# Kernel optimization log

Hardware: AMD Instinct MI355X
Metric: run time of the kernel (lower is better)

## Reference

```python
import jax, jax.numpy as jnp
import numpy as np

WS = 3  # window size


def _shift_stack(t_pad, D, H, W):
    # t_pad: [B, nh, hd, D+2p, H+2p, W+2p] -> [B, nh, hd, D, H, W, WS**3]
    slabs = [t_pad[..., i:i + D, j:j + H, l:l + W]
             for i in range(WS) for j in range(WS) for l in range(WS)]
    return jnp.stack(slabs, axis=-1)


def setup_inputs() -> dict:
    key = jax.random.key(0)
    ks = jax.random.split(key, 6)
    B, C, D, H, W = 2, 128, 24, 24, 24
    nh, hd = 4, 32
    return {
        "x": jax.random.normal(ks[0], (B, C, D, H, W), dtype=jnp.float32),
        "qkv_w": jax.random.normal(ks[1], (3 * C, C), dtype=jnp.float32) * 0.02,
        "qkv_b": jax.random.normal(ks[2], (3 * C,), dtype=jnp.float32) * 0.02,
        "proj_w": jax.random.normal(ks[3], (C, C), dtype=jnp.float32) * 0.02,
        "proj_b": jax.random.normal(ks[4], (C,), dtype=jnp.float32) * 0.02,
        "pos_embed": jax.random.normal(ks[5], (hd, WS, WS, WS), dtype=jnp.float32) * 0.02,
    }


def reference(x, qkv_w, qkv_b, proj_w, proj_b, pos_embed):
    B, C, D, H, W = x.shape
    hd = pos_embed.shape[0]
    nh = C // hd
    scale = hd ** -0.5
    pad = WS // 2

    # 1x1x1 Conv3d == pointwise linear over channel dim
    qkv = jnp.einsum('bcdhw,oc->bodhw', x, qkv_w) + qkv_b[None, :, None, None, None]
    q, k, v = jnp.split(qkv, 3, axis=1)
    q = q.reshape(B, nh, hd, D, H, W)
    k = k.reshape(B, nh, hd, D, H, W)
    v = v.reshape(B, nh, hd, D, H, W)

    pcfg = [(0, 0)] * 3 + [(pad, pad)] * 3
    k_pad = jnp.pad(k, pcfg)
    v_pad = jnp.pad(v, pcfg)

    # windows: [B, nh, hd, D, H, W, WS^3]; window center of q == q itself
    k_win = _shift_stack(k_pad, D, H, W)
    v_win = _shift_stack(v_pad, D, H, W)
    k_win = k_win + pos_embed.reshape(hd, WS ** 3)[None, None, :, None, None, None, :]

    scores = jnp.einsum('bncdhw,bncdhwk->bndhwk', q, k_win) * scale
    attn = jax.nn.softmax(scores, axis=-1)
    out = jnp.einsum('bndhwk,bncdhwk->bncdhw', attn, v_win)
    out = out.reshape(B, C, D, H, W)
    return jnp.einsum('bcdhw,oc->bodhw', out, proj_w) + proj_b[None, :, None, None, None]
```

## Files before the change

### kernel.cpp

```cpp
#include <hip/hip_runtime.h>
#include <hip/hip_bf16.h>

#define SVOX 13824
#define CIN 128
#define NHEAD 4
#define HDIM 32

#define BD 2
#define BH 4
#define BW 8
#define WD (BD+2)
#define WH (BH+2)
#define WW (BW+2)
#define NWIN (WD*WH*WW)

typedef __attribute__((ext_vector_type(8))) short short8;
typedef __attribute__((ext_vector_type(4))) float f32x4;
#if defined(__has_builtin)
#if __has_builtin(__builtin_amdgcn_fdot2_f32_bf16)
#define HAVE_DOT2BF 1
typedef __attribute__((ext_vector_type(2))) __bf16 bf16x2;
#endif
#if __has_builtin(__builtin_amdgcn_mov_dpp)
#define HAVE_DPP 1
#endif
#endif

__device__ __forceinline__ unsigned short f2bf(float x) {
    unsigned u = __float_as_uint(x);
    u += 0x7FFFu + ((u >> 16) & 1u);
    return (unsigned short)(u >> 16);
}
__device__ __forceinline__ float dot2bf(unsigned a, unsigned b, float c) {
#ifdef HAVE_DOT2BF
    return __builtin_amdgcn_fdot2_f32_bf16(__builtin_bit_cast(bf16x2, a),
                                           __builtin_bit_cast(bf16x2, b), c, false);
#else
    return __uint_as_float(a << 16) * __uint_as_float(b << 16)
         + __uint_as_float(a & 0xffff0000u) * __uint_as_float(b & 0xffff0000u) + c;
#endif
}
template<int CTRL>
__device__ __forceinline__ float quad_dpp(float x) {
#ifdef HAVE_DPP
    return __int_as_float(__builtin_amdgcn_mov_dpp(__float_as_int(x), CTRL, 0xf, 0xf, true));
#else
    return __shfl_xor(x, (CTRL == 0xB1) ? 1 : 2);
#endif
}

__global__ __launch_bounds__(256) void qkv_gemm(
    const float* __restrict__ X,
    const float* __restrict__ W,
    const float* __restrict__ bias,
    const float* __restrict__ pos,
    unsigned* __restrict__ pe_out,
    ushort* __restrict__ q_out,
    ushort* __restrict__ k_out,
    ushort* __restrict__ v_out)
{
    __shared__ __align__(16) unsigned char smem[26624];
    ushort* Wb = (ushort*)smem;
    ushort* Xs = (ushort*)(smem + 17408);
    float*  T  = (float*)smem;

    const int t    = threadIdx.x;
    const int s0   = blockIdx.x * 64;
    const int o0   = blockIdx.y * 64;
    const int b    = blockIdx.z;
    const int lane = t & 63;
    const int wid  = t >> 6;
    const int l15  = lane & 15;
    const int g4   = lane >> 4;
    const int wm   = (wid >> 1) * 32;
    const int wn   = (wid & 1) * 32;

    if (blockIdx.x == 0 && blockIdx.y == 0 && blockIdx.z == 0 && t < 27 * 16) {
        int w = t >> 4, cp = t & 15;
        unsigned lo = f2bf(pos[(2 * cp) * 27 + w]);
        unsigned hi = f2bf(pos[(2 * cp + 1) * 27 + w]);
        pe_out[t] = lo | (hi << 16);
    }

    #pragma unroll
    for (int i = 0; i < 8; i++) {
        int f = t + i * 256;
        int row = f >> 5, c4 = f & 31;
        float4 w = *(const float4*)(W + (size_t)(o0 + row) * CIN + c4 * 4);
        ushort4 u;
        u.x = f2bf(w.x); u.y = f2bf(w.y); u.z = f2bf(w.z); u.w = f2bf(w.w);
        *(ushort4*)(Wb + row * 136 + c4 * 4) = u;
    }

    f32x4 acc[2][2];
    #pragma unroll
    for (int mf = 0; mf < 2; mf++)
        #pragma unroll
        for (int nf = 0; nf < 2; nf++)
            acc[mf][nf] = (f32x4){0.f, 0.f, 0.f, 0.f};

    const int sx = t & 63;
    const int kg = t >> 6;

    for (int chunk = 0; chunk < 2; chunk++) {
        __syncthreads();
        ushort xk[16];
        #pragma unroll
        for (int i = 0; i < 16; i++) {
            int k = kg * 16 + i;
            xk[i] = f2bf(X[((size_t)b * CIN + chunk * 64 + k) * SVOX + s0 + sx]);
        }
        #pragma unroll
        for (int j = 0; j < 2; j++) {
            short8 v;
            #pragma unroll
            for (int e = 0; e < 8; e++) v[e] = (short)xk[j * 8 + e];
            *(short8*)(Xs + sx * 72 + kg * 16 + j * 8) = v;
        }
        __syncthreads();

        #pragma unroll
        for (int ks = 0; ks < 2; ks++) {
            short8 Af[2], Bf[2];
            #pragma unroll
            for (int mf = 0; mf < 2; mf++)
                Af[mf] = *(const short8*)(Wb + (wm + mf * 16 + l15) * 136 + chunk * 64 + ks * 32 + g4 * 8);
            #pragma unroll
            for (int nf = 0; nf < 2; nf++)
                Bf[nf] = *(const short8*)(Xs + (wn + nf * 16 + l15) * 72 + ks * 32 + g4 * 8);
            #pragma unroll
            for (int mf = 0; mf < 2; mf++)
                #pragma unroll
                for (int nf = 0; nf < 2; nf++)
                    acc[mf][nf] = __builtin_amdgcn_mfma_f32_16x16x32_bf16(Af[mf], Bf[nf], acc[mf][nf], 0, 0, 0);
        }
    }

    __syncthreads();
    #pragma unroll
    for (int mf = 0; mf < 2; mf++)
        #pragma unroll
        for (int nf = 0; nf < 2; nf++) {
            int s  = wn + nf * 16 + l15;
            int mb = wm + mf * 16 + g4 * 4;
            *(f32x4*)(T + s * 68 + mb) = acc[mf][nf];
        }
    __syncthreads();
    #pragma unroll
    for (int i = 0; i < 4; i++) {
        int f = t + i * 256;
        int og = f & 15, sl = f >> 4;
        float4 v = *(float4*)(T + sl * 68 + og * 4);
        int o_g = o0 + og * 4;
        v.x += bias[o_g]; v.y += bias[o_g + 1]; v.z += bias[o_g + 2]; v.w += bias[o_g + 3];
        int part = o_g >> 7, pc = o_g & 127;
        int head = pc >> 5, ic = pc & 31;
        size_t base = (((size_t)b * NHEAD + head) * SVOX + s0 + sl) * HDIM + ic;
        ushort4 u;
        u.x = f2bf(v.x); u.y = f2bf(v.y); u.z = f2bf(v.z); u.w = f2bf(v.w);
        ushort* dst = (part == 0) ? q_out : (part == 1) ? k_out : v_out;
        *(ushort4*)(dst + base) = u;
    }
}

__global__ __launch_bounds__(256, 5) void attn_kernel(
    const ushort* __restrict__ qbf,
    const ushort* __restrict__ kbf,
    const ushort* __restrict__ vbf,
    const unsigned* __restrict__ pe_g,
    ushort* __restrict__ aout)
{
    __shared__ __align__(16) ushort Kl[NWIN * 32];
    __shared__ __align__(16) ushort Vl[NWIN * 32];

    const int t = threadIdx.x;
    const int br = blockIdx.x;
    const int n  = blockIdx.y;
    const int b  = blockIdx.z;
    const int bw_ = br % 3;
    const int bh_ = (br / 3) % 6;
    const int bd_ = br / 18;
    const int d0 = bd_ * BD, h0 = bh_ * BH, w0 = bw_ * BW;

    const ushort* kb = kbf + ((size_t)b * NHEAD + n) * (size_t)SVOX * HDIM;
    const ushort* vb = vbf + ((size_t)b * NHEAD + n) * (size_t)SVOX * HDIM;

    #pragma unroll
    for (int i = 0; i < 4; i++) {
        int f = t + i * 256;
        if (f < NWIN * 4) {
            int u = f >> 2, ch = f & 3;
            int ud = u / (WH * WW);
            int r  = u - ud * (WH * WW);
            int uh = r / WW;
            int uw = r - uh * WW;
            int gd = d0 + ud - 1, gh = h0 + uh - 1, gw = w0 + uw - 1;
            bool valid = ((unsigned)gd < 24u) & ((unsigned)gh < 24u) & ((unsigned)gw < 24u);
            size_t gsv = valid ? (size_t)(gd * 576 + gh * 24 + gw) : 0;
            uint4 kv = *(const uint4*)(kb + gsv * HDIM + ch * 8);
            uint4 vv = *(const uint4*)(vb + gsv * HDIM + ch * 8);
            if (!valid) { kv = make_uint4(0,0,0,0); vv = make_uint4(0,0,0,0); }
            *(uint4*)(Kl + u * 32 + ch * 8) = kv;
            *(uint4*)(Vl + u * 32 + ch * 8) = vv;
        }
    }

    const int p   = t >> 2;
    const int sub = t & 3;
    const int pw = p & 7, ph = (p >> 3) & 3, pd = p >> 5;
    const int dd0 = d0 + pd, hh0 = h0 + ph, ww0 = w0 + pw;
    const int sv = dd0 * 576 + hh0 * 24 + ww0;
    uint4 qpk = *(const uint4*)(qbf + (((size_t)b * NHEAD + n) * SVOX + sv) * HDIM + sub * 8);

    unsigned vm = 0;
    {
        int widx = 0;
        #pragma unroll
        for (int di = -1; di <= 1; di++)
        #pragma unroll
        for (int dj = -1; dj <= 1; dj++)
        #pragma unroll
        for (int dl = -1; dl <= 1; dl++) {
            if (((unsigned)(dd0 + di) < 24u) & ((unsigned)(hh0 + dj) < 24u) & ((unsigned)(ww0 + dl) < 24u))
                vm |= 1u << widx;
            widx++;
        }
    }
    (void)vm;

    float sc[27];
    #pragma unroll
    for (int s = 0; s < 27; s++) {
        uint4 pp = *(const uint4*)(pe_g + s * 16 + sub * 4);
        float a = dot2bf(qpk.x, pp.x, 0.f);
        a = dot2bf(qpk.y, pp.y, a);
        a = dot2bf(qpk.z, pp.z, a);
        a = dot2bf(qpk.w, pp.w, a);
        sc[s] = a;
    }

    __syncthreads();

    const int wc = (pd + 1) * (WH * WW) + (ph + 1) * WW + (pw + 1);
    const ushort* Kbase = Kl + wc * 32 + sub * 8;

    #pragma unroll
    for (int s = 0; s < 27; s++) {
        const int di = s / 9 - 1, dj = (s / 3) % 3 - 1, dl = s % 3 - 1;
        const int off = (di * (WH * WW) + dj * WW + dl) * 32;
        uint4 kk = *(const uint4*)(Kbase + off);
        float a = sc[s];
        a = dot2bf(qpk.x, kk.x, a);
        a = dot2bf(qpk.y, kk.y, a);
        a = dot2bf(qpk.z, kk.z, a);
        a = dot2bf(qpk.w, kk.w, a);
        sc[s] = a;
    }

    #pragma unroll
    for (int s = 0; s < 27; s++) {
        sc[s] += quad_dpp<0xB1>(sc[s]);
        sc[s] += quad_dpp<0x4E>(sc[s]);
    }

    const float scale = 0.17677669529663687f;
    float mx = -1e30f;
    #pragma unroll
    for (int s = 0; s < 27; s++) {
        sc[s] *= scale;
        mx = fmaxf(mx, sc[s]);
    }
    float sum = 0.f;
    #pragma unroll
    for (int s = 0; s < 27; s++) {
        float e = __expf(sc[s] - mx);
        sc[s] = e;
        sum += e;
    }
    float inv = 1.f / sum;

    const ushort* Vbase = Vl + wc * 32 + sub * 8;
    float o[8];
    #pragma unroll
    for (int i = 0; i < 8; i++) o[i] = 0.f;
    #pragma unroll
    for (int s = 0; s < 27; s++) {
        const int di = s / 9 - 1, dj = (s / 3) % 3 - 1, dl = s % 3 - 1;
        const int off = (di * (WH * WW) + dj * WW + dl) * 32;
        uint4 vv = *(const uint4*)(Vbase + off);
        float pr = sc[s];
        o[0] += pr * __uint_as_float(vv.x << 16);
        o[1] += pr * __uint_as_float(vv.x & 0xffff0000u);
        o[2] += pr * __uint_as_float(vv.y << 16);
        o[3] += pr * __uint_as_float(vv.y & 0xffff0000u);
        o[4] += pr * __uint_as_float(vv.z << 16);
        o[5] += pr * __uint_as_float(vv.z & 0xffff0000u);
        o[6] += pr * __uint_as_float(vv.w << 16);
        o[7] += pr * __uint_as_float(vv.w & 0xffff0000u);
    }

    uint4 ou;
    ou.x = (unsigned)f2bf(o[0] * inv) | ((unsigned)f2bf(o[1] * inv) << 16);
    ou.y = (unsigned)f2bf(o[2] * inv) | ((unsigned)f2bf(o[3] * inv) << 16);
    ou.z = (unsigned)f2bf(o[4] * inv) | ((unsigned)f2bf(o[5] * inv) << 16);
    ou.w = (unsigned)f2bf(o[6] * inv) | ((unsigned)f2bf(o[7] * inv) << 16);
    *(uint4*)(aout + ((size_t)b * SVOX + sv) * CIN + n * HDIM + sub * 8) = ou;
}

__global__ __launch_bounds__(256) void proj_gemm(
    const ushort* __restrict__ Xa,
    const float* __restrict__ W,
    const float* __restrict__ bias,
    float* __restrict__ out)
{
    __shared__ __align__(16) unsigned char smem[34816];
    ushort* Wb = (ushort*)smem;
    ushort* Xs = (ushort*)(smem + 17408);
    float*  T  = (float*)smem;

    const int t    = threadIdx.x;
    const int s0   = blockIdx.x * 64;
    const int o0   = blockIdx.y * 64;
    const int b    = blockIdx.z;
    const int lane = t & 63;
    const int wid  = t >> 6;
    const int l15  = lane & 15;
    const int g4   = lane >> 4;
    const int wm   = (wid >> 1) * 32;
    const int wn   = (wid & 1) * 32;

    #pragma unroll
    for (int i = 0; i < 8; i++) {
        int f = t + i * 256;
        int row = f >> 5, c4 = f & 31;
        float4 w = *(const float4*)(W + (size_t)(o0 + row) * CIN + c4 * 4);
        ushort4 u;
        u.x = f2bf(w.x); u.y = f2bf(w.y); u.z = f2bf(w.z); u.w = f2bf(w.w);
        *(ushort4*)(Wb + row * 136 + c4 * 4) = u;
    }
    #pragma unroll
    for (int i = 0; i < 4; i++) {
        int f = t + i * 256;
        int row = f >> 4, c8 = f & 15;
        *(uint4*)(Xs + row * 136 + c8 * 8) =
            *(const uint4*)(Xa + ((size_t)b * SVOX + s0 + row) * CIN + c8 * 8);
    }
    __syncthreads();

    f32x4 acc[2][2];
    #pragma unroll
    for (int mf = 0; mf < 2; mf++)
        #pragma unroll
        for (int nf = 0; nf < 2; nf++)
            acc[mf][nf] = (f32x4){0.f, 0.f, 0.f, 0.f};

    #pragma unroll
    for (int ks = 0; ks < 4; ks++) {
        short8 Af[2], Bf[2];
        #pragma unroll
        for (int mf = 0; mf < 2; mf++)
            Af[mf] = *(const short8*)(Wb + (wm + mf * 16 + l15) * 136 + ks * 32 + g4 * 8);
        #pragma unroll
        for (int nf = 0; nf < 2; nf++)
            Bf[nf] = *(const short8*)(Xs + (wn + nf * 16 + l15) * 136 + ks * 32 + g4 * 8);
        #pragma unroll
        for (int mf = 0; mf < 2; mf++)
            #pragma unroll
            for (int nf = 0; nf < 2; nf++)
                acc[mf][nf] = __builtin_amdgcn_mfma_f32_16x16x32_bf16(Af[mf], Bf[nf], acc[mf][nf], 0, 0, 0);
    }

    __syncthreads();
    #pragma unroll
    for (int mf = 0; mf < 2; mf++)
        #pragma unroll
        for (int nf = 0; nf < 2; nf++) {
            int s  = wn + nf * 16 + l15;
            int mb = wm + mf * 16 + g4 * 4;
            #pragma unroll
            for (int r = 0; r < 4; r++)
                T[(mb + r) * 72 + s] = acc[mf][nf][r];
        }
    __syncthreads();
    #pragma unroll
    for (int i = 0; i < 4; i++) {
        int f = t + i * 256;
        int s4 = f & 15, m = f >> 4;
        float4 v = *(float4*)(T + m * 72 + s4 * 4);
        float bi = bias[o0 + m];
        v.x += bi; v.y += bi; v.z += bi; v.w += bi;
        *(float4*)(out + ((size_t)b * CIN + o0 + m) * SVOX + s0 + s4 * 4) = v;
    }
}

extern "C" void kernel_launch(void* const* d_in, const int* in_sizes, int n_in,
                              void* d_out, int out_size, void* d_ws, size_t ws_size,
                              hipStream_t stream) {
    const float* x      = (const float*)d_in[0];
    const float* qkv_w  = (const float*)d_in[1];
    const float* qkv_b  = (const float*)d_in[2];
    const float* proj_w = (const float*)d_in[3];
    const float* proj_b = (const float*)d_in[4];
    const float* pos    = (const float*)d_in[5];
    float* out = (float*)d_out;

    const size_t HSZ = (size_t)2 * NHEAD * SVOX * HDIM;
    ushort* qb  = (ushort*)d_ws;
    ushort* kbp = qb + HSZ;
    ushort* vbp = kbp + HSZ;
    ushort* attn_o = vbp + HSZ;
    unsigned* pe_p = (unsigned*)(attn_o + HSZ);

    qkv_gemm<<<dim3(SVOX/64, 384/64, 2), 256, 0, stream>>>(x, qkv_w, qkv_b, pos, pe_p, qb, kbp, vbp);
    attn_kernel<<<dim3(216, NHEAD, 2), 256, 0, stream>>>(qb, kbp, vbp, pe_p, attn_o);
    proj_gemm<<<dim3(SVOX/64, CIN/64, 2), 256, 0, stream>>>(attn_o, proj_w, proj_b, out);
}
```

Baseline: 46.94 us.

## Pre-convert weights to bf16 once and enlarge GEMM output tiles

Adds a prep kernel that converts the qkv and proj weights and the positional embedding to bf16 once, so the GEMM blocks copy bf16 weights directly instead of each converting fp32. The qkv GEMM now computes 192 output channels per block (grid y drops from 6 to 2), so each X tile is loaded and converted fewer times. The proj GEMM now covers 128 voxels per block. In exchange it adds an extra kernel launch and much more LDS per block (60KB for qkv), which lowers occupancy and cuts the block count.

```diff
diff --git a/kernel.cpp b/kernel.cpp
--- a/kernel.cpp
+++ b/kernel.cpp
@@ -49,54 +49,76 @@
 #endif
 }
 
+__global__ __launch_bounds__(256) void prep_kernel(
+    const float* __restrict__ qkv_w,
+    const float* __restrict__ proj_w,
+    const float* __restrict__ pos,
+    ushort* __restrict__ Wq,
+    ushort* __restrict__ Wp,
+    unsigned* __restrict__ pe)
+{
+    int id = blockIdx.x * 256 + threadIdx.x;
+    if (id < 6144) {
+        float4 a = *(const float4*)(qkv_w + (size_t)id * 8);
+        float4 b = *(const float4*)(qkv_w + (size_t)id * 8 + 4);
+        ushort4 u, v;
+        u.x = f2bf(a.x); u.y = f2bf(a.y); u.z = f2bf(a.z); u.w = f2bf(a.w);
+        v.x = f2bf(b.x); v.y = f2bf(b.y); v.z = f2bf(b.z); v.w = f2bf(b.w);
+        *(ushort4*)(Wq + (size_t)id * 8) = u;
+        *(ushort4*)(Wq + (size_t)id * 8 + 4) = v;
+    } else if (id < 8192) {
+        int j = id - 6144;
+        float4 a = *(const float4*)(proj_w + (size_t)j * 8);
+        float4 b = *(const float4*)(proj_w + (size_t)j * 8 + 4);
+        ushort4 u, v;
+        u.x = f2bf(a.x); u.y = f2bf(a.y); u.z = f2bf(a.z); u.w = f2bf(a.w);
+        v.x = f2bf(b.x); v.y = f2bf(b.y); v.z = f2bf(b.z); v.w = f2bf(b.w);
+        *(ushort4*)(Wp + (size_t)j * 8) = u;
+        *(ushort4*)(Wp + (size_t)j * 8 + 4) = v;
+    } else if (id < 8192 + 432) {
+        int j = id - 8192;
+        int w = j >> 4, cp = j & 15;
+        unsigned lo = f2bf(pos[(2 * cp) * 27 + w]);
+        unsigned hi = f2bf(pos[(2 * cp + 1) * 27 + w]);
+        pe[j] = lo | (hi << 16);
+    }
+}
+
 __global__ __launch_bounds__(256) void qkv_gemm(
     const float* __restrict__ X,
-    const float* __restrict__ W,
+    const ushort* __restrict__ Wg,
     const float* __restrict__ bias,
-    const float* __restrict__ pos,
-    unsigned* __restrict__ pe_out,
     ushort* __restrict__ q_out,
     ushort* __restrict__ k_out,
     ushort* __restrict__ v_out)
 {
-    __shared__ __align__(16) unsigned char smem[26624];
+    __shared__ __align__(16) unsigned char smem[61440];
     ushort* Wb = (ushort*)smem;
-    ushort* Xs = (ushort*)(smem + 17408);
+    ushort* Xs = (ushort*)(smem + 52224);
     float*  T  = (float*)smem;
 
     const int t    = threadIdx.x;
     const int s0   = blockIdx.x * 64;
-    const int o0   = blockIdx.y * 64;
+    const int o0   = blockIdx.y * 192;
     const int b    = blockIdx.z;
     const int lane = t & 63;
     const int wid  = t >> 6;
     const int l15  = lane & 15;
     const int g4   = lane >> 4;
-    const int wm   = (wid >> 1) * 32;
-    const int wn   = (wid & 1) * 32;
-
-    if (blockIdx.x == 0 && blockIdx.y == 0 && blockIdx.z == 0 && t < 27 * 16) {
-        int w = t >> 4, cp = t & 15;
-        unsigned lo = f2bf(pos[(2 * cp) * 27 + w]);
-        unsigned hi = f2bf(pos[(2 * cp + 1) * 27 + w]);
-        pe_out[t] = lo | (hi << 16);
-    }
-
-    #pragma unroll
-    for (int i = 0; i < 8; i++) {
+
+    #pragma unroll
+    for (int i = 0; i < 12; i++) {
         int f = t + i * 256;
-        int row = f >> 5, c4 = f & 31;
-        float4 w = *(const float4*)(W + (size_t)(o0 + row) * CIN + c4 * 4);
-        ushort4 u;
-        u.x = f2bf(w.x); u.y = f2bf(w.y); u.z = f2bf(w.z); u.w = f2bf(w.w);
-        *(ushort4*)(Wb + row * 136 + c4 * 4) = u;
-    }
-
-    f32x4 acc[2][2];
-    #pragma unroll
-    for (int mf = 0; mf < 2; mf++)
-        #pragma unroll
-        for (int nf = 0; nf < 2; nf++)
+        int row = f >> 4, c8 = f & 15;
+        *(uint4*)(Wb + row * 136 + c8 * 8) =
+            *(const uint4*)(Wg + (size_t)(o0 + row) * CIN + c8 * 8);
+    }
+
+    f32x4 acc[3][4];
+    #pragma unroll
+    for (int mf = 0; mf < 3; mf++)
+        #pragma unroll
+        for (int nf = 0; nf < 4; nf++)
             acc[mf][nf] = (f32x4){0.f, 0.f, 0.f, 0.f};
 
     const int sx = t & 63;
@@ -121,45 +143,43 @@
 
         #pragma unroll
         for (int ks = 0; ks < 2; ks++) {
-            short8 Af[2], Bf[2];
-            #pragma unroll
-            for (int mf = 0; mf < 2; mf++)
-                Af[mf] = *(const short8*)(Wb + (wm + mf * 16 + l15) * 136 + chunk * 64 + ks * 32 + g4 * 8);
-            #pragma unroll
-            for (int nf = 0; nf < 2; nf++)
-                Bf[nf] = *(const short8*)(Xs + (wn + nf * 16 + l15) * 72 + ks * 32 + g4 * 8);
-            #pragma unroll
-            for (int mf = 0; mf < 2; mf++)
+            short8 Bf[4], Af[3];
+            #pragma unroll
+            for (int nf = 0; nf < 4; nf++)
+                Bf[nf] = *(const short8*)(Xs + (nf * 16 + l15) * 72 + ks * 32 + g4 * 8);
+            #pragma unroll
+            for (int mf = 0; mf < 3; mf++)
+                Af[mf] = *(const short8*)(Wb + (mf * 64 + wid * 16 + l15) * 136 + chunk * 64 + ks * 32 + g4 * 8);
+            #pragma unroll
+            for (int mf = 0; mf < 3; mf++)
                 #pragma unroll
-                for (int nf = 0; nf < 2; nf++)
+                for (int nf = 0; nf < 4; nf++)
                     acc[mf][nf] = __builtin_amdgcn_mfma_f32_16x16x32_bf16(Af[mf], Bf[nf], acc[mf][nf], 0, 0, 0);
         }
     }
 
-    __syncthreads();
-    #pragma unroll
-    for (int mf = 0; mf < 2; mf++)
-        #pragma unroll
-        for (int nf = 0; nf < 2; nf++) {
-            int s  = wn + nf * 16 + l15;
-            int mb = wm + mf * 16 + g4 * 4;
-            *(f32x4*)(T + s * 68 + mb) = acc[mf][nf];
-        }
-    __syncthreads();
-    #pragma unroll
-    for (int i = 0; i < 4; i++) {
-        int f = t + i * 256;
-        int og = f & 15, sl = f >> 4;
-        float4 v = *(float4*)(T + sl * 68 + og * 4);
-        int o_g = o0 + og * 4;
-        v.x += bias[o_g]; v.y += bias[o_g + 1]; v.z += bias[o_g + 2]; v.w += bias[o_g + 3];
-        int part = o_g >> 7, pc = o_g & 127;
-        int head = pc >> 5, ic = pc & 31;
-        size_t base = (((size_t)b * NHEAD + head) * SVOX + s0 + sl) * HDIM + ic;
-        ushort4 u;
-        u.x = f2bf(v.x); u.y = f2bf(v.y); u.z = f2bf(v.z); u.w = f2bf(v.w);
-        ushort* dst = (part == 0) ? q_out : (part == 1) ? k_out : v_out;
-        *(ushort4*)(dst + base) = u;
+    #pragma unroll
+    for (int p = 0; p < 3; p++) {
+        __syncthreads();
+        #pragma unroll
+        for (int nf = 0; nf < 4; nf++)
+            *(f32x4*)(T + (nf * 16 + l15) * 68 + wid * 16 + g4 * 4) = acc[p][nf];
+        __syncthreads();
+        #pragma unroll
+        for (int i = 0; i < 4; i++) {
+            int f = t + i * 256;
+            int og = f & 15, sl = f >> 4;
+            float4 v = *(float4*)(T + sl * 68 + og * 4);
+            int o_g = o0 + p * 64 + og * 4;
+            v.x += bias[o_g]; v.y += bias[o_g + 1]; v.z += bias[o_g + 2]; v.w += bias[o_g + 3];
+            int part = o_g >> 7, pc = o_g & 127;
+            int head = pc >> 5, ic = pc & 31;
+            size_t base = (((size_t)b * NHEAD + head) * SVOX + s0 + sl) * HDIM + ic;
+            ushort4 u;
+            u.x = f2bf(v.x); u.y = f2bf(v.y); u.z = f2bf(v.z); u.w = f2bf(v.w);
+            ushort* dst = (part == 0) ? q_out : (part == 1) ? k_out : v_out;
+            *(ushort4*)(dst + base) = u;
+        }
     }
 }
 
@@ -212,22 +232,6 @@
     const int sv = dd0 * 576 + hh0 * 24 + ww0;
     uint4 qpk = *(const uint4*)(qbf + (((size_t)b * NHEAD + n) * SVOX + sv) * HDIM + sub * 8);
 
-    unsigned vm = 0;
-    {
-        int widx = 0;
-        #pragma unroll
-        for (int di = -1; di <= 1; di++)
-        #pragma unroll
-        for (int dj = -1; dj <= 1; dj++)
-        #pragma unroll
-        for (int dl = -1; dl <= 1; dl++) {
-            if (((unsigned)(dd0 + di) < 24u) & ((unsigned)(hh0 + dj) < 24u) & ((unsigned)(ww0 + dl) < 24u))
-                vm |= 1u << widx;
-            widx++;
-        }
-    }
-    (void)vm;
-
     float sc[27];
     #pragma unroll
     for (int s = 0; s < 27; s++) {
@@ -309,37 +313,35 @@
 
 __global__ __launch_bounds__(256) void proj_gemm(
     const ushort* __restrict__ Xa,
-    const float* __restrict__ W,
+    const ushort* __restrict__ Wg,
     const float* __restrict__ bias,
     float* __restrict__ out)
 {
-    __shared__ __align__(16) unsigned char smem[34816];
+    __shared__ __align__(16) unsigned char smem[52224];
     ushort* Wb = (ushort*)smem;
     ushort* Xs = (ushort*)(smem + 17408);
     float*  T  = (float*)smem;
 
     const int t    = threadIdx.x;
-    const int s0   = blockIdx.x * 64;
+    const int s0   = blockIdx.x * 128;
     const int o0   = blockIdx.y * 64;
     const int b    = blockIdx.z;
     const int lane = t & 63;
     const int wid  = t >> 6;
     const int l15  = lane & 15;
     const int g4   = lane >> 4;
-    const int wm   = (wid >> 1) * 32;
-    const int wn   = (wid & 1) * 32;
-
+    const int wo   = (wid & 1) * 32;
+    const int ws   = (wid >> 1) * 64;
+
+    #pragma unroll
+    for (int i = 0; i < 4; i++) {
+        int f = t + i * 256;
+        int row = f >> 4, c8 = f & 15;
+        *(uint4*)(Wb + row * 136 + c8 * 8) =
+            *(const uint4*)(Wg + (size_t)(o0 + row) * CIN + c8 * 8);
+    }
     #pragma unroll
     for (int i = 0; i < 8; i++) {
-        int f = t + i * 256;
-        int row = f >> 5, c4 = f & 31;
-        float4 w = *(const float4*)(W + (size_t)(o0 + row) * CIN + c4 * 4);
-        ushort4 u;
-        u.x = f2bf(w.x); u.y = f2bf(w.y); u.z = f2bf(w.z); u.w = f2bf(w.w);
-        *(ushort4*)(Wb + row * 136 + c4 * 4) = u;
-    }
-    #pragma unroll
-    for (int i = 0; i < 4; i++) {
         int f = t + i * 256;
         int row = f >> 4, c8 = f & 15;
         *(uint4*)(Xs + row * 136 + c8 * 8) =
@@ -347,26 +349,26 @@
     }
     __syncthreads();
 
-    f32x4 acc[2][2];
+    f32x4 acc[2][4];
     #pragma unroll
     for (int mf = 0; mf < 2; mf++)
         #pragma unroll
-        for (int nf = 0; nf < 2; nf++)
+        for (int nf = 0; nf < 4; nf++)
             acc[mf][nf] = (f32x4){0.f, 0.f, 0.f, 0.f};
 
     #pragma unroll
     for (int ks = 0; ks < 4; ks++) {
-        short8 Af[2], Bf[2];
+        short8 Af[2], Bf[4];
         #pragma unroll
         for (int mf = 0; mf < 2; mf++)
-            Af[mf] = *(const short8*)(Wb + (wm + mf * 16 + l15) * 136 + ks * 32 + g4 * 8);
-        #pragma unroll
-        for (int nf = 0; nf < 2; nf++)
-            Bf[nf] = *(const short8*)(Xs + (wn + nf * 16 + l15) * 136 + ks * 32 + g4 * 8);
+            Af[mf] = *(const short8*)(Wb + (wo + mf * 16 + l15) * 136 + ks * 32 + g4 * 8);
+        #pragma unroll
+        for (int nf = 0; nf < 4; nf++)
+            Bf[nf] = *(const short8*)(Xs + (ws + nf * 16 + l15) * 136 + ks * 32 + g4 * 8);
         #pragma unroll
         for (int mf = 0; mf < 2; mf++)
             #pragma unroll
-            for (int nf = 0; nf < 2; nf++)
+            for (int nf = 0; nf < 4; nf++)
                 acc[mf][nf] = __builtin_amdgcn_mfma_f32_16x16x32_bf16(Af[mf], Bf[nf], acc[mf][nf], 0, 0, 0);
     }
 
@@ -374,19 +376,19 @@
     #pragma unroll
     for (int mf = 0; mf < 2; mf++)
         #pragma unroll
-        for (int nf = 0; nf < 2; nf++) {
-            int s  = wn + nf * 16 + l15;
-            int mb = wm + mf * 16 + g4 * 4;
+        for (int nf = 0; nf < 4; nf++) {
+            int s  = ws + nf * 16 + l15;
+            int mb = wo + mf * 16 + g4 * 4;
             #pragma unroll
             for (int r = 0; r < 4; r++)
-                T[(mb + r) * 72 + s] = acc[mf][nf][r];
+                T[(mb + r) * 132 + s] = acc[mf][nf][r];
         }
     __syncthreads();
     #pragma unroll
-    for (int i = 0; i < 4; i++) {
+    for (int i = 0; i < 8; i++) {
         int f = t + i * 256;
-        int s4 = f & 15, m = f >> 4;
-        float4 v = *(float4*)(T + m * 72 + s4 * 4);
+        int s4 = f & 31, m = f >> 5;
+        float4 v = *(float4*)(T + m * 132 + s4 * 4);
         float bi = bias[o0 + m];
         v.x += bi; v.y += bi; v.z += bi; v.w += bi;
         *(float4*)(out + ((size_t)b * CIN + o0 + m) * SVOX + s0 + s4 * 4) = v;
@@ -409,9 +411,12 @@
     ushort* kbp = qb + HSZ;
     ushort* vbp = kbp + HSZ;
     ushort* attn_o = vbp + HSZ;
-    unsigned* pe_p = (unsigned*)(attn_o + HSZ);
-
-    qkv_gemm<<<dim3(SVOX/64, 384/64, 2), 256, 0, stream>>>(x, qkv_w, qkv_b, pos, pe_p, qb, kbp, vbp);
+    ushort* Wq  = attn_o + HSZ;
+    ushort* Wp  = Wq + 384 * CIN;
+    unsigned* pe_p = (unsigned*)(Wp + CIN * CIN);
+
+    prep_kernel<<<34, 256, 0, stream>>>(qkv_w, proj_w, pos, Wq, Wp, pe_p);
+    qkv_gemm<<<dim3(SVOX/64, 2, 2), 256, 0, stream>>>(x, Wq, qkv_b, qb, kbp, vbp);
     attn_kernel<<<dim3(216, NHEAD, 2), 256, 0, stream>>>(qb, kbp, vbp, pe_p, attn_o);
-    proj_gemm<<<dim3(SVOX/64, CIN/64, 2), 256, 0, stream>>>(attn_o, proj_w, proj_b, out);
-}
+    proj_gemm<<<dim3(SVOX/128, 2, 2), 256, 0, stream>>>(attn_o, Wp, proj_b, out);
+}
```

Measured after the change: 49.89 us. +6.3%, slower.

## Store V in fp16 and accumulate attention output with packed half FMAs

Applied to the files above, without the earlier changes.

The QKV GEMM now writes V as fp16 instead of bf16, and the attention kernel accumulates P·V with packed __hfma2 on half2 registers instead of unpacking bf16 to fp32 and doing scalar FMAs. This roughly halves the ALU work in the PV loop. Softmax is also restructured: a tree max reduction and exp2f with the scale folded into the log2e constant, and an unused validity mask is removed. Accumulating in fp16 lowers precision and risks overflow if V values are large.

```diff
diff --git a/kernel.cpp b/kernel.cpp
--- a/kernel.cpp
+++ b/kernel.cpp
@@ -1,5 +1,6 @@
 #include <hip/hip_runtime.h>
 #include <hip/hip_bf16.h>
+#include <hip/hip_fp16.h>
 
 #define SVOX 13824
 #define CIN 128
@@ -24,6 +25,9 @@
 #if __has_builtin(__builtin_amdgcn_mov_dpp)
 #define HAVE_DPP 1
 #endif
+#if __has_builtin(__builtin_amdgcn_cvt_pkrtz)
+#define HAVE_PKRTZ 1
+#endif
 #endif
 
 __device__ __forceinline__ unsigned short f2bf(float x) {
@@ -47,6 +51,20 @@
 #else
     return __shfl_xor(x, (CTRL == 0xB1) ? 1 : 2);
 #endif
+}
+__device__ __forceinline__ __half2 u2h2(unsigned u) {
+    union { unsigned u; __half2 h; } c; c.u = u; return c.h;
+}
+__device__ __forceinline__ __half2 splat_h2(float x) {
+#ifdef HAVE_PKRTZ
+    auto v = __builtin_amdgcn_cvt_pkrtz(x, x);
+    union { decltype(v) a; __half2 h; } c; c.a = v; return c.h;
+#else
+    return __float2half2_rn(x);
+#endif
+}
+__device__ __forceinline__ unsigned short f2h(float x) {
+    return __builtin_bit_cast(unsigned short, (_Float16)x);
 }
 
 __global__ __launch_bounds__(256) void qkv_gemm(
@@ -157,7 +175,11 @@
         int head = pc >> 5, ic = pc & 31;
         size_t base = (((size_t)b * NHEAD + head) * SVOX + s0 + sl) * HDIM + ic;
         ushort4 u;
-        u.x = f2bf(v.x); u.y = f2bf(v.y); u.z = f2bf(v.z); u.w = f2bf(v.w);
+        if (part == 2) {
+            u.x = f2h(v.x); u.y = f2h(v.y); u.z = f2h(v.z); u.w = f2h(v.w);
+        } else {
+            u.x = f2bf(v.x); u.y = f2bf(v.y); u.z = f2bf(v.z); u.w = f2bf(v.w);
+        }
         ushort* dst = (part == 0) ? q_out : (part == 1) ? k_out : v_out;
         *(ushort4*)(dst + base) = u;
     }
@@ -166,7 +188,7 @@
 __global__ __launch_bounds__(256, 5) void attn_kernel(
     const ushort* __restrict__ qbf,
     const ushort* __restrict__ kbf,
-    const ushort* __restrict__ vbf,
+    const ushort* __restrict__ vhf,
     const unsigned* __restrict__ pe_g,
     ushort* __restrict__ aout)
 {
@@ -183,7 +205,7 @@
     const int d0 = bd_ * BD, h0 = bh_ * BH, w0 = bw_ * BW;
 
     const ushort* kb = kbf + ((size_t)b * NHEAD + n) * (size_t)SVOX * HDIM;
-    const ushort* vb = vbf + ((size_t)b * NHEAD + n) * (size_t)SVOX * HDIM;
+    const ushort* vb = vhf + ((size_t)b * NHEAD + n) * (size_t)SVOX * HDIM;
 
     #pragma unroll
     for (int i = 0; i < 4; i++) {
@@ -208,25 +230,8 @@
     const int p   = t >> 2;
     const int sub = t & 3;
     const int pw = p & 7, ph = (p >> 3) & 3, pd = p >> 5;
-    const int dd0 = d0 + pd, hh0 = h0 + ph, ww0 = w0 + pw;
-    const int sv = dd0 * 576 + hh0 * 24 + ww0;
+    const int sv = (d0 + pd) * 576 + (h0 + ph) * 24 + w0 + pw;
     uint4 qpk = *(const uint4*)(qbf + (((size_t)b * NHEAD + n) * SVOX + sv) * HDIM + sub * 8);
-
-    unsigned vm = 0;
-    {
-        int widx = 0;
-        #pragma unroll
-        for (int di = -1; di <= 1; di++)
-        #pragma unroll
-        for (int dj = -1; dj <= 1; dj++)
-        #pragma unroll
-        for (int dl = -1; dl <= 1; dl++) {
-            if (((unsigned)(dd0 + di) < 24u) & ((unsigned)(hh0 + dj) < 24u) & ((unsigned)(ww0 + dl) < 24u))
-                vm |= 1u << widx;
-            widx++;
-        }
-    }
-    (void)vm;
 
     float sc[27];
     #pragma unroll
@@ -263,40 +268,46 @@
         sc[s] += quad_dpp<0x4E>(sc[s]);
     }
 
-    const float scale = 0.17677669529663687f;
-    float mx = -1e30f;
+    float m3[9];
+    #pragma unroll
+    for (int j = 0; j < 9; j++)
+        m3[j] = fmaxf(fmaxf(sc[3*j], sc[3*j+1]), sc[3*j+2]);
+    float m9a = fmaxf(fmaxf(m3[0], m3[1]), m3[2]);
+    float m9b = fmaxf(fmaxf(m3[3], m3[4]), m3[5]);
+    float m9c = fmaxf(fmaxf(m3[6], m3[7]), m3[8]);
+    float mx  = fmaxf(fmaxf(m9a, m9b), m9c);
+
+    const float KS = 0.17677669529663687f * 1.4426950408889634f;
+    float sum = 0.f;
     #pragma unroll
     for (int s = 0; s < 27; s++) {
-        sc[s] *= scale;
-        mx = fmaxf(mx, sc[s]);
-    }
-    float sum = 0.f;
-    #pragma unroll
-    for (int s = 0; s < 27; s++) {
-        float e = __expf(sc[s] - mx);
+        float e = exp2f((sc[s] - mx) * KS);
         sc[s] = e;
         sum += e;
     }
     float inv = 1.f / sum;
 
     const ushort* Vbase = Vl + wc * 32 + sub * 8;
-    float o[8];
-    #pragma unroll
-    for (int i = 0; i < 8; i++) o[i] = 0.f;
+    __half2 o2[4];
+    __half2 hz = __float2half2_rn(0.f);
+    o2[0] = hz; o2[1] = hz; o2[2] = hz; o2[3] = hz;
     #pragma unroll
     for (int s = 0; s < 27; s++) {
         const int di = s / 9 - 1, dj = (s / 3) % 3 - 1, dl = s % 3 - 1;
         const int off = (di * (WH * WW) + dj * WW + dl) * 32;
         uint4 vv = *(const uint4*)(Vbase + off);
-        float pr = sc[s];
-        o[0] += pr * __uint_as_float(vv.x << 16);
-        o[1] += pr * __uint_as_float(vv.x & 0xffff0000u);
-        o[2] += pr * __uint_as_float(vv.y << 16);
-        o[3] += pr * __uint_as_float(vv.y & 0xffff0000u);
-        o[4] += pr * __uint_as_float(vv.z << 16);
-        o[5] += pr * __uint_as_float(vv.z & 0xffff0000u);
-        o[6] += pr * __uint_as_float(vv.w << 16);
-        o[7] += pr * __uint_as_float(vv.w & 0xffff0000u);
+        __half2 p2 = splat_h2(sc[s]);
+        o2[0] = __hfma2(p2, u2h2(vv.x), o2[0]);
+        o2[1] = __hfma2(p2, u2h2(vv.y), o2[1]);
+        o2[2] = __hfma2(p2, u2h2(vv.z), o2[2]);
+        o2[3] = __hfma2(p2, u2h2(vv.w), o2[3]);
+    }
+
+    float o[8];
+    #pragma unroll
+    for (int j = 0; j < 4; j++) {
+        o[2*j]   = __low2float(o2[j]);
+        o[2*j+1] = __high2float(o2[j]);
     }
 
     uint4 ou;
```

Measured after the change: 46.32 us. About the same (-1.3%).
